# Kernel optimization log

Measured on AMD Instinct MI355X. Metric: run time of the kernel, lower is better.

The kernel has to match this reference:

```python
import jax, jax.numpy as jnp
import numpy as np

B, T, D = 4, 2048, 2048
H = 16
NOPE, ROPE, VD = 64, 64, 128
QK = NOPE + ROPE  # 128
KV_R, Q_R = 512, 1024
EPS = 1e-6
THETA = 10000.0
SCALE = 1.0 / np.sqrt(QK)


def rmsnorm(x, g):
    var = jnp.mean(jnp.square(x), axis=-1, keepdims=True)
    return x * jax.lax.rsqrt(var + EPS) * g


def rope_tables(seq_len, dim):
    inv_freq = 1.0 / (THETA ** (np.arange(0, dim, 2, dtype=np.float32) / dim))
    t = np.arange(seq_len, dtype=np.float32)
    freqs = np.outer(t, inv_freq)              # [T, dim/2]
    emb = np.concatenate([freqs, freqs], -1)   # [T, dim]
    return jnp.asarray(np.cos(emb)), jnp.asarray(np.sin(emb))


def rotate_half(x):
    x1, x2 = jnp.split(x, 2, axis=-1)
    return jnp.concatenate([-x2, x1], axis=-1)


def apply_rope(x, cos, sin):
    # x: [B,H,S,dim]; cos/sin: [S,dim] -> broadcast over B,H
    return x * cos[None, None] + rotate_half(x) * sin[None, None]


def setup_inputs() -> dict:
    key = jax.random.key(0)
    ks = jax.random.split(key, 10)
    w = lambda k, shp: jax.random.normal(k, shp, jnp.float32) * 0.02
    return {
        'x': jax.random.normal(ks[0], (B, T, D), jnp.float32),
        'w_q_down': w(ks[1], (D, Q_R)),
        'g_q_down': jnp.ones((Q_R,), jnp.float32),
        'w_q_up': w(ks[2], (Q_R, H * QK)),
        'w_kv_down': w(ks[3], (D, KV_R)),
        'g_kv_down': jnp.ones((KV_R,), jnp.float32),
        'w_k_up': w(ks[4], (KV_R, H * NOPE)),
        'w_v_up': w(ks[5], (KV_R, H * VD)),
        'w_k_rope': w(ks[6], (D, ROPE)),
        'g_q': jnp.ones((QK,), jnp.float32),
        'g_k': jnp.ones((QK,), jnp.float32),
        'w_gate': w(ks[7], (D, H * VD)),
        'w_o': w(ks[8], (H * VD, D)),
    }


def reference(x, w_q_down, g_q_down, w_q_up, w_kv_down, g_kv_down,
              w_k_up, w_v_up, w_k_rope, g_q, g_k, w_gate, w_o):
    cos, sin = rope_tables(T, ROPE)

    # Low-rank Q: down-proj -> RMSNorm -> up-proj
    q_c = rmsnorm(x @ w_q_down, g_q_down)                       # [B,T,Q_R]
    q = (q_c @ w_q_up).reshape(B, T, H, QK).transpose(0, 2, 1, 3)  # [B,H,T,QK]
    q_nope, q_rope = q[..., :NOPE], q[..., NOPE:]

    # Low-rank KV compression
    c_kv = rmsnorm(x @ w_kv_down, g_kv_down)                    # [B,S,KV_R]
    k_rope = x @ w_k_rope                                       # [B,S,ROPE]
    S = T
    k_nope = (c_kv @ w_k_up).reshape(B, S, H, NOPE).transpose(0, 2, 1, 3)
    v = (c_kv @ w_v_up).reshape(B, S, H, VD).transpose(0, 2, 1, 3)

    # Decoupled RoPE: shared k_rope broadcast over heads
    k_rope = jnp.broadcast_to(k_rope[:, None], (B, H, S, ROPE))
    q_rope = apply_rope(q_rope, cos[:T], sin[:T])
    k_rope = apply_rope(k_rope, cos[:S], sin[:S])

    q = rmsnorm(jnp.concatenate([q_nope, q_rope], -1), g_q)     # [B,H,T,QK]
    k = rmsnorm(jnp.concatenate([k_nope, k_rope], -1), g_k)     # [B,H,S,QK]

    # Causal SDPA
    scores = jnp.einsum('bhtd,bhsd->bhts', q, k) * SCALE
    mask = jnp.tril(jnp.ones((T, S), bool))
    scores = jnp.where(mask, scores, jnp.finfo(scores.dtype).min)
    attn = jax.nn.softmax(scores, axis=-1)
    out = jnp.einsum('bhts,bhsd->bhtd', attn, v)                # [B,H,T,VD]

    # Gating
    gate = (x @ w_gate).reshape(B, T, H, VD).transpose(0, 2, 1, 3)
    out = out * jax.nn.silu(gate)

    out = out.transpose(0, 2, 1, 3).reshape(B, T, H * VD)
    return out @ w_o
```

## Files before the change

kernel.cpp:

```cpp
#include <hip/hip_runtime.h>
#include <hip/hip_bf16.h>
#include <math.h>

typedef __bf16 bf16_t;
typedef __bf16 bf16x8 __attribute__((ext_vector_type(8)));
typedef float f32x4 __attribute__((ext_vector_type(4)));

#define SCALE_F 0.08838834764831845f
#define SMAX_F 14.0f

#define GLOAD_LDS16(gp, lp)                                              \
    __builtin_amdgcn_global_load_lds(                                    \
        (const __attribute__((address_space(1))) void*)(gp),             \
        (__attribute__((address_space(3))) void*)(lp), 16, 0, 0)

__global__ void k_convert(const float* __restrict__ in, bf16_t* __restrict__ out, int n) {
    int i = (blockIdx.x * 256 + threadIdx.x) * 4;
    if (i >= n) return;
    float4 f = *(const float4*)(in + i);
    out[i + 0] = (bf16_t)f.x;
    out[i + 1] = (bf16_t)f.y;
    out[i + 2] = (bf16_t)f.z;
    out[i + 3] = (bf16_t)f.w;
}

__global__ void k_transpose(const float* __restrict__ w, bf16_t* __restrict__ wt, int K, int N) {
    __shared__ float tile[32][33];
    int n0 = blockIdx.x * 32, k0 = blockIdx.y * 32;
    int tx = threadIdx.x & 31, ty = threadIdx.x >> 5;
#pragma unroll
    for (int i = 0; i < 32; i += 8)
        tile[ty + i][tx] = w[(size_t)(k0 + ty + i) * N + (n0 + tx)];
    __syncthreads();
#pragma unroll
    for (int i = 0; i < 32; i += 8)
        wt[(size_t)(n0 + ty + i) * K + (k0 + tx)] = (bf16_t)tile[tx][ty + i];
}

__global__ void k_rope_tables(float* __restrict__ cosT, float* __restrict__ sinT) {
    int idx = blockIdx.x * 256 + threadIdx.x;
    int t = idx >> 6, i = idx & 63;
    float invf = powf(10000.f, -(float)(i & 31) / 32.f);
    float ang = (float)t * invf;
    float s, c;
    sincosf(ang, &s, &c);
    cosT[idx] = c;
    sinT[idx] = s;
}

__global__ void k_rmsnorm(bf16_t* __restrict__ x, const float* __restrict__ g, int C) {
    bf16_t* p = x + (size_t)blockIdx.x * C;
    float ss = 0.f;
    for (int i = threadIdx.x; i < C; i += 256) {
        float v = (float)p[i];
        ss += v * v;
    }
#pragma unroll
    for (int m = 32; m; m >>= 1) ss += __shfl_xor(ss, m);
    __shared__ float red[4];
    if ((threadIdx.x & 63) == 0) red[threadIdx.x >> 6] = ss;
    __syncthreads();
    float tot = red[0] + red[1] + red[2] + red[3];
    float scale = rsqrtf(tot / (float)C + 1e-6f);
    for (int i = threadIdx.x; i < C; i += 256)
        p[i] = (bf16_t)((float)p[i] * scale * g[i]);
}

template <int OUTF32>
__global__ __launch_bounds__(256) void k_gemm(const bf16_t* __restrict__ A,
                                              const bf16_t* __restrict__ Bt,
                                              void* __restrict__ Cp, int M, int N, int K,
                                              size_t sA, size_t sB, size_t sC) {
    __shared__ bf16_t As[128 * 32];
    __shared__ bf16_t Bs[128 * 32];
    A += (size_t)blockIdx.z * sA;
    Bt += (size_t)blockIdx.z * sB;
    const size_t coff = (size_t)blockIdx.z * sC;
    const int bm = blockIdx.y * 128, bn = blockIdx.x * 128;
    const int tid = threadIdx.x, lane = tid & 63, wv = tid >> 6;
    const int quad = lane >> 4, l16 = lane & 15;
    const int wm = (wv >> 1) * 64, wn = (wv & 1) * 64;
    f32x4 acc[4][4] = {};
    const int sr0 = wv * 32 + (lane >> 2);
    const int scc = (lane & 3) * 8;
    bf16_t* ldsA0 = As + (wv * 2) * 512;
    bf16_t* ldsA1 = As + (wv * 2 + 1) * 512;
    bf16_t* ldsB0 = Bs + (wv * 2) * 512;
    bf16_t* ldsB1 = Bs + (wv * 2 + 1) * 512;
    const bool bok0 = (bn + sr0) < N;
    const bool bok1 = (bn + sr0 + 16) < N;
    for (int k0 = 0; k0 < K; k0 += 32) {
        const bf16_t* gA = A + (size_t)(bm + sr0) * K + k0 + scc;
        const bf16_t* gB = Bt + (size_t)(bn + sr0) * K + k0 + scc;
        GLOAD_LDS16(gA, ldsA0);
        GLOAD_LDS16(gA + (size_t)16 * K, ldsA1);
        if (bok0) GLOAD_LDS16(gB, ldsB0);
        if (bok1) GLOAD_LDS16(gB + (size_t)16 * K, ldsB1);
        __syncthreads();
        bf16x8 af[4], bfr[4];
#pragma unroll
        for (int mi = 0; mi < 4; ++mi)
            af[mi] = *(bf16x8*)(As + (wm + mi * 16 + l16) * 32 + quad * 8);
#pragma unroll
        for (int ni = 0; ni < 4; ++ni)
            bfr[ni] = *(bf16x8*)(Bs + (wn + ni * 16 + l16) * 32 + quad * 8);
#pragma unroll
        for (int mi = 0; mi < 4; ++mi)
#pragma unroll
            for (int ni = 0; ni < 4; ++ni)
                acc[mi][ni] =
                    __builtin_amdgcn_mfma_f32_16x16x32_bf16(af[mi], bfr[ni], acc[mi][ni], 0, 0, 0);
        __syncthreads();
    }
#pragma unroll
    for (int mi = 0; mi < 4; ++mi)
#pragma unroll
        for (int ni = 0; ni < 4; ++ni)
#pragma unroll
            for (int r = 0; r < 4; ++r) {
                int row = bm + wm + mi * 16 + quad * 4 + r;
                int col = bn + wn + ni * 16 + l16;
                if (col < N) {
                    if constexpr (OUTF32)
                        ((float*)Cp)[coff + (size_t)row * N + col] = acc[mi][ni][r];
                    else
                        ((bf16_t*)Cp)[coff + (size_t)row * N + col] = (bf16_t)acc[mi][ni][r];
                }
            }
}

__global__ void k_build_q(bf16_t* __restrict__ q, const float* __restrict__ g,
                          const float* __restrict__ cosT, const float* __restrict__ sinT) {
    int wid = blockIdx.x * 4 + (threadIdx.x >> 6);
    int lane = threadIdx.x & 63;
    int row = wid >> 4, h = wid & 15;
    int t = row & 2047;
    bf16_t* p = q + (size_t)row * 2048 + h * 128;
    float x0 = (float)p[lane];
    float x1 = (float)p[64 + lane];
    float xp = (float)p[64 + (lane ^ 32)];
    float c = cosT[t * 64 + lane], s = sinT[t * 64 + lane];
    float rot = (lane < 32) ? -xp : xp;
    float y1 = x1 * c + rot * s;
    float ss = x0 * x0 + y1 * y1;
#pragma unroll
    for (int m = 32; m; m >>= 1) ss += __shfl_xor(ss, m);
    float scale = rsqrtf(ss / 128.f + 1e-6f);
    p[lane] = (bf16_t)(x0 * scale * g[lane]);
    p[64 + lane] = (bf16_t)(y1 * scale * g[64 + lane]);
}

__global__ void k_build_k(const bf16_t* __restrict__ knope, const bf16_t* __restrict__ krope,
                          bf16_t* __restrict__ kout, const float* __restrict__ g,
                          const float* __restrict__ cosT, const float* __restrict__ sinT) {
    int wid = blockIdx.x * 4 + (threadIdx.x >> 6);
    int lane = threadIdx.x & 63;
    int row = wid >> 4, h = wid & 15;
    int t = row & 2047;
    float x0 = (float)knope[(size_t)row * 1024 + h * 64 + lane];
    float x1 = (float)krope[(size_t)row * 64 + lane];
    float xp = (float)krope[(size_t)row * 64 + (lane ^ 32)];
    float c = cosT[t * 64 + lane], s = sinT[t * 64 + lane];
    float rot = (lane < 32) ? -xp : xp;
    float y1 = x1 * c + rot * s;
    float ss = x0 * x0 + y1 * y1;
#pragma unroll
    for (int m = 32; m; m >>= 1) ss += __shfl_xor(ss, m);
    float scale = rsqrtf(ss / 128.f + 1e-6f);
    bf16_t* p = kout + (size_t)row * 2048 + h * 128;
    p[lane] = (bf16_t)(x0 * scale * g[lane]);
    p[64 + lane] = (bf16_t)(y1 * scale * g[64 + lane]);
}

__global__ __launch_bounds__(512, 4) void k_attn(const bf16_t* __restrict__ q,
                                                 const bf16_t* __restrict__ k,
                                                 const bf16_t* __restrict__ vT,
                                                 const bf16_t* __restrict__ gate,
                                                 bf16_t* __restrict__ o) {
    __shared__ bf16_t Ks[64 * 136];
    __shared__ bf16_t Vt[128 * 72];
    __shared__ bf16_t Ps[128 * 72];
    const int qb = (int)gridDim.x - 1 - (int)blockIdx.x;
    const int bh = blockIdx.y;
    const int b = bh >> 4, h = bh & 15;
    const int t0 = qb * 128;
    const int tid = threadIdx.x, lane = tid & 63, wv = tid >> 6;
    const int quad = lane >> 4, l16 = lane & 15;
    const int wrow = t0 + wv * 16;

    bf16x8 aq[4];
    {
        const bf16_t* qp = q + ((size_t)(b * 2048 + wrow + l16)) * 2048 + h * 128 + quad * 8;
#pragma unroll
        for (int kk = 0; kk < 4; ++kk) aq[kk] = *(const bf16x8*)(qp + kk * 32);
    }
    f32x4 oacc[8] = {};
    float l_i[4] = {0.f, 0.f, 0.f, 0.f};

    const bf16_t* vbase = vT + ((size_t)b * 2048 + (size_t)h * 128) * 2048;
    const bf16_t* kbase = k + ((size_t)b * 2048) * 2048 + h * 128;

    const int krow = tid >> 4;
    const int kcol = (tid & 15) * 8;
    const int vrow = tid >> 3;
    const int vcol = (tid & 7) * 8;

    const int nkb = 2 * qb + 2;
    bf16x8 kreg0, kreg1, vreg0, vreg1;
    {
        kreg0 = *(const bf16x8*)(kbase + (size_t)krow * 2048 + kcol);
        kreg1 = *(const bf16x8*)(kbase + (size_t)(krow + 32) * 2048 + kcol);
        vreg0 = *(const bf16x8*)(vbase + (size_t)vrow * 2048 + vcol);
        vreg1 = *(const bf16x8*)(vbase + (size_t)(vrow + 64) * 2048 + vcol);
    }
    for (int kb = 0; kb < nkb; ++kb) {
        const int s0 = kb * 64;
        __syncthreads();
        *(bf16x8*)(Ks + krow * 136 + kcol) = kreg0;
        *(bf16x8*)(Ks + (krow + 32) * 136 + kcol) = kreg1;
        *(bf16x8*)(Vt + vrow * 72 + vcol) = vreg0;
        *(bf16x8*)(Vt + (vrow + 64) * 72 + vcol) = vreg1;
        __syncthreads();
        if (kb + 1 < nkb) {
            const int sn = s0 + 64;
            kreg0 = *(const bf16x8*)(kbase + (size_t)(sn + krow) * 2048 + kcol);
            kreg1 = *(const bf16x8*)(kbase + (size_t)(sn + krow + 32) * 2048 + kcol);
            vreg0 = *(const bf16x8*)(vbase + (size_t)vrow * 2048 + sn + vcol);
            vreg1 = *(const bf16x8*)(vbase + (size_t)(vrow + 64) * 2048 + sn + vcol);
        }
        if (s0 > wrow + 15) continue;
        f32x4 sc[4] = {};
#pragma unroll
        for (int kk = 0; kk < 4; ++kk)
#pragma unroll
            for (int ni = 0; ni < 4; ++ni) {
                bf16x8 bk = *(bf16x8*)(Ks + (ni * 16 + l16) * 136 + kk * 32 + quad * 8);
                sc[ni] = __builtin_amdgcn_mfma_f32_16x16x32_bf16(aq[kk], bk, sc[ni], 0, 0, 0);
            }
        const bool diag = (s0 + 63 > wrow);
        const int trowb = wrow + quad * 4;
#pragma unroll
        for (int ni = 0; ni < 4; ++ni) {
            int scol = s0 + ni * 16 + l16;
#pragma unroll
            for (int r2 = 0; r2 < 4; ++r2) {
                float pv = __expf(sc[ni][r2] * SCALE_F - SMAX_F);
                if (diag && scol > trowb + r2) pv = 0.f;
                sc[ni][r2] = pv;
                l_i[r2] += pv;
            }
        }
#pragma unroll
        for (int ni = 0; ni < 4; ++ni)
#pragma unroll
            for (int r2 = 0; r2 < 4; ++r2)
                Ps[(wv * 16 + quad * 4 + r2) * 72 + ni * 16 + l16] = (bf16_t)sc[ni][r2];
#pragma unroll
        for (int kk = 0; kk < 2; ++kk) {
            bf16x8 ap = *(bf16x8*)(Ps + (wv * 16 + l16) * 72 + kk * 32 + quad * 8);
#pragma unroll
            for (int ni = 0; ni < 8; ++ni) {
                bf16x8 bv = *(bf16x8*)(Vt + (ni * 16 + l16) * 72 + kk * 32 + quad * 8);
                oacc[ni] = __builtin_amdgcn_mfma_f32_16x16x32_bf16(ap, bv, oacc[ni], 0, 0, 0);
            }
        }
    }
#pragma unroll
    for (int m = 8; m; m >>= 1)
#pragma unroll
        for (int r2 = 0; r2 < 4; ++r2) l_i[r2] += __shfl_xor(l_i[r2], m);
    float rl[4];
#pragma unroll
    for (int r2 = 0; r2 < 4; ++r2) rl[r2] = 1.f / l_i[r2];
#pragma unroll
    for (int ni = 0; ni < 8; ++ni) {
        int d = ni * 16 + l16;
#pragma unroll
        for (int r2 = 0; r2 < 4; ++r2) {
            int trow = wrow + quad * 4 + r2;
            size_t gi = ((size_t)(b * 2048 + trow)) * 2048 + h * 128 + d;
            float gt = (float)gate[gi];
            float sg = gt / (1.f + __expf(-gt));
            o[gi] = (bf16_t)((oacc[ni][r2] * rl[r2]) * sg);
        }
    }
}

extern "C" void kernel_launch(void* const* d_in, const int* in_sizes, int n_in,
                              void* d_out, int out_size, void* d_ws, size_t ws_size,
                              hipStream_t stream) {
    const float* x         = (const float*)d_in[0];
    const float* w_q_down  = (const float*)d_in[1];
    const float* g_q_down  = (const float*)d_in[2];
    const float* w_q_up    = (const float*)d_in[3];
    const float* w_kv_down = (const float*)d_in[4];
    const float* g_kv_down = (const float*)d_in[5];
    const float* w_k_up    = (const float*)d_in[6];
    const float* w_v_up    = (const float*)d_in[7];
    const float* w_k_rope  = (const float*)d_in[8];
    const float* g_q       = (const float*)d_in[9];
    const float* g_k       = (const float*)d_in[10];
    const float* w_gate    = (const float*)d_in[11];
    const float* w_o       = (const float*)d_in[12];
    float* out = (float*)d_out;

    char* base = (char*)d_ws;
    size_t off = 0;
    auto alloc = [&](size_t bytes) -> void* {
        void* p = base + off;
        off = (off + bytes + 255) & ~(size_t)255;
        return p;
    };
    const size_t MT = 8192;
    bf16_t* xb     = (bf16_t*)alloc(MT * 2048 * 2);
    bf16_t* wqd_t  = (bf16_t*)alloc((size_t)1024 * 2048 * 2);
    bf16_t* wqu_t  = (bf16_t*)alloc((size_t)2048 * 1024 * 2);
    bf16_t* wkvd_t = (bf16_t*)alloc((size_t)512 * 2048 * 2);
    bf16_t* wku_t  = (bf16_t*)alloc((size_t)1024 * 512 * 2);
    bf16_t* wvu_t  = (bf16_t*)alloc((size_t)2048 * 512 * 2);
    bf16_t* wkr_t  = (bf16_t*)alloc((size_t)64 * 2048 * 2);
    bf16_t* wg_t   = (bf16_t*)alloc((size_t)2048 * 2048 * 2);
    bf16_t* wo_t   = (bf16_t*)alloc((size_t)2048 * 2048 * 2);
    bf16_t* qc     = (bf16_t*)alloc(MT * 1024 * 2);
    bf16_t* ckv    = (bf16_t*)alloc(MT * 512 * 2);
    bf16_t* krope  = (bf16_t*)alloc(MT * 64 * 2);
    bf16_t* vT     = (bf16_t*)alloc(MT * 2048 * 2);
    bf16_t* gbuf   = (bf16_t*)alloc(MT * 2048 * 2);
    float* cosT    = (float*)alloc((size_t)2048 * 64 * 4);
    float* sinT    = (float*)alloc((size_t)2048 * 64 * 4);
    bf16_t* knope = qc;
    bf16_t* qbuf  = (bf16_t*)d_out;
    bf16_t* kbuf  = (bf16_t*)d_out + MT * 2048;
    bf16_t* obuf  = xb;

    k_convert<<<dim3(16384), dim3(256), 0, stream>>>(x, xb, 16777216);
    k_transpose<<<dim3(32, 64), 256, 0, stream>>>(w_q_down, wqd_t, 2048, 1024);
    k_transpose<<<dim3(64, 32), 256, 0, stream>>>(w_q_up, wqu_t, 1024, 2048);
    k_transpose<<<dim3(16, 64), 256, 0, stream>>>(w_kv_down, wkvd_t, 2048, 512);
    k_transpose<<<dim3(32, 16), 256, 0, stream>>>(w_k_up, wku_t, 512, 1024);
    k_transpose<<<dim3(64, 16), 256, 0, stream>>>(w_v_up, wvu_t, 512, 2048);
    k_transpose<<<dim3(2, 64), 256, 0, stream>>>(w_k_rope, wkr_t, 2048, 64);
    k_transpose<<<dim3(64, 64), 256, 0, stream>>>(w_gate, wg_t, 2048, 2048);
    k_transpose<<<dim3(64, 64), 256, 0, stream>>>(w_o, wo_t, 2048, 2048);
    k_rope_tables<<<dim3(512), 256, 0, stream>>>(cosT, sinT);
    k_gemm<0><<<dim3(8, 64), 256, 0, stream>>>(xb, wqd_t, qc, 8192, 1024, 2048, 0, 0, 0);
    k_rmsnorm<<<dim3(8192), 256, 0, stream>>>(qc, g_q_down, 1024);
    k_gemm<0><<<dim3(16, 64), 256, 0, stream>>>(qc, wqu_t, qbuf, 8192, 2048, 1024, 0, 0, 0);
    k_gemm<0><<<dim3(4, 64), 256, 0, stream>>>(xb, wkvd_t, ckv, 8192, 512, 2048, 0, 0, 0);
    k_rmsnorm<<<dim3(8192), 256, 0, stream>>>(ckv, g_kv_down, 512);
    k_gemm<0><<<dim3(8, 64), 256, 0, stream>>>(ckv, wku_t, knope, 8192, 1024, 512, 0, 0, 0);
    k_gemm<0><<<dim3(16, 16, 4), 256, 0, stream>>>(wvu_t, ckv, vT, 2048, 2048, 512,
                                                   0, (size_t)2048 * 512, (size_t)2048 * 2048);
    k_gemm<0><<<dim3(1, 64), 256, 0, stream>>>(xb, wkr_t, krope, 8192, 64, 2048, 0, 0, 0);
    k_gemm<0><<<dim3(16, 64), 256, 0, stream>>>(xb, wg_t, gbuf, 8192, 2048, 2048, 0, 0, 0);
    k_build_q<<<dim3(32768), 256, 0, stream>>>(qbuf, g_q, cosT, sinT);
    k_build_k<<<dim3(32768), 256, 0, stream>>>(knope, krope, kbuf, g_k, cosT, sinT);
    k_attn<<<dim3(16, 64), 512, 0, stream>>>(qbuf, kbuf, vT, gbuf, obuf);
    k_gemm<1><<<dim3(16, 64), 256, 0, stream>>>(obuf, wo_t, out, 8192, 2048, 2048, 0, 0, 0);
}
```

Baseline: 850.5 us.

## Split attention waves into 32-row by key/dim halves with XOR-swizzled LDS

The attention kernel now gives each pair of waves a 32-row query tile. The two waves split the key columns for QK^T and the value dimensions for PV, so each LDS fragment of K or V feeds two MFMAs instead of one. Padded LDS rows are replaced with an XOR swizzle to avoid bank conflicts while shrinking shared memory. The change adds an extra block barrier per key tile and an LDS reduction of the row sums across wave pairs, and each wave now computes some fully masked rows on the diagonal.

```diff
diff --git a/kernel.cpp b/kernel.cpp
--- a/kernel.cpp
+++ b/kernel.cpp
@@ -177,33 +177,40 @@
                                                  const bf16_t* __restrict__ vT,
                                                  const bf16_t* __restrict__ gate,
                                                  bf16_t* __restrict__ o) {
-    __shared__ bf16_t Ks[64 * 136];
-    __shared__ bf16_t Vt[128 * 72];
-    __shared__ bf16_t Ps[128 * 72];
+    __shared__ bf16_t Ks[64 * 128];
+    __shared__ bf16_t Vt[128 * 64];
+    __shared__ bf16_t Ps[128 * 64];
     const int qb = (int)gridDim.x - 1 - (int)blockIdx.x;
     const int bh = blockIdx.y;
     const int b = bh >> 4, h = bh & 15;
     const int t0 = qb * 128;
     const int tid = threadIdx.x, lane = tid & 63, wv = tid >> 6;
     const int quad = lane >> 4, l16 = lane & 15;
-    const int wrow = t0 + wv * 16;
-
-    bf16x8 aq[4];
-    {
-        const bf16_t* qp = q + ((size_t)(b * 2048 + wrow + l16)) * 2048 + h * 128 + quad * 8;
-#pragma unroll
-        for (int kk = 0; kk < 4; ++kk) aq[kk] = *(const bf16x8*)(qp + kk * 32);
-    }
-    f32x4 oacc[8] = {};
-    float l_i[4] = {0.f, 0.f, 0.f, 0.f};
+    const int wt = wv >> 1;
+    const int part = wv & 1;
+    const int wrow = t0 + wt * 32;
+    const int swl = (l16 & 7) << 3;
+
+    bf16x8 aq[2][4];
+#pragma unroll
+    for (int mi = 0; mi < 2; ++mi) {
+        const bf16_t* qp =
+            q + ((size_t)(b * 2048 + wrow + mi * 16 + l16)) * 2048 + h * 128 + quad * 8;
+#pragma unroll
+        for (int kk = 0; kk < 4; ++kk) aq[mi][kk] = *(const bf16x8*)(qp + kk * 32);
+    }
+    f32x4 oacc[2][4] = {};
+    float l_i[2][4] = {};
 
     const bf16_t* vbase = vT + ((size_t)b * 2048 + (size_t)h * 128) * 2048;
     const bf16_t* kbase = k + ((size_t)b * 2048) * 2048 + h * 128;
 
     const int krow = tid >> 4;
     const int kcol = (tid & 15) * 8;
+    const int kdst = krow * 128 + (kcol ^ ((krow & 7) << 3));
     const int vrow = tid >> 3;
     const int vcol = (tid & 7) * 8;
+    const int vdst = vrow * 64 + (vcol ^ ((vrow & 7) << 3));
 
     const int nkb = 2 * qb + 2;
     bf16x8 kreg0, kreg1, vreg0, vreg1;
@@ -216,10 +223,10 @@
     for (int kb = 0; kb < nkb; ++kb) {
         const int s0 = kb * 64;
         __syncthreads();
-        *(bf16x8*)(Ks + krow * 136 + kcol) = kreg0;
-        *(bf16x8*)(Ks + (krow + 32) * 136 + kcol) = kreg1;
-        *(bf16x8*)(Vt + vrow * 72 + vcol) = vreg0;
-        *(bf16x8*)(Vt + (vrow + 64) * 72 + vcol) = vreg1;
+        *(bf16x8*)(Ks + kdst) = kreg0;
+        *(bf16x8*)(Ks + kdst + 32 * 128) = kreg1;
+        *(bf16x8*)(Vt + vdst) = vreg0;
+        *(bf16x8*)(Vt + vdst + 64 * 64) = vreg1;
         __syncthreads();
         if (kb + 1 < nkb) {
             const int sn = s0 + 64;
@@ -228,61 +235,94 @@
             vreg0 = *(const bf16x8*)(vbase + (size_t)vrow * 2048 + sn + vcol);
             vreg1 = *(const bf16x8*)(vbase + (size_t)(vrow + 64) * 2048 + sn + vcol);
         }
-        if (s0 > wrow + 15) continue;
-        f32x4 sc[4] = {};
-#pragma unroll
-        for (int kk = 0; kk < 4; ++kk)
-#pragma unroll
-            for (int ni = 0; ni < 4; ++ni) {
-                bf16x8 bk = *(bf16x8*)(Ks + (ni * 16 + l16) * 136 + kk * 32 + quad * 8);
-                sc[ni] = __builtin_amdgcn_mfma_f32_16x16x32_bf16(aq[kk], bk, sc[ni], 0, 0, 0);
-            }
-        const bool diag = (s0 + 63 > wrow);
-        const int trowb = wrow + quad * 4;
-#pragma unroll
-        for (int ni = 0; ni < 4; ++ni) {
-            int scol = s0 + ni * 16 + l16;
-#pragma unroll
-            for (int r2 = 0; r2 < 4; ++r2) {
-                float pv = __expf(sc[ni][r2] * SCALE_F - SMAX_F);
-                if (diag && scol > trowb + r2) pv = 0.f;
-                sc[ni][r2] = pv;
-                l_i[r2] += pv;
+        const bool active = (s0 <= wrow + 31);
+        if (active) {
+#pragma unroll
+            for (int ni = 0; ni < 2; ++ni) {
+                f32x4 sc2[2] = {{0.f, 0.f, 0.f, 0.f}, {0.f, 0.f, 0.f, 0.f}};
+#pragma unroll
+                for (int kk = 0; kk < 4; ++kk) {
+                    bf16x8 bk = *(bf16x8*)(Ks + (part * 32 + ni * 16 + l16) * 128 +
+                                           ((kk * 32 + quad * 8) ^ swl));
+                    sc2[0] = __builtin_amdgcn_mfma_f32_16x16x32_bf16(aq[0][kk], bk, sc2[0], 0, 0, 0);
+                    sc2[1] = __builtin_amdgcn_mfma_f32_16x16x32_bf16(aq[1][kk], bk, sc2[1], 0, 0, 0);
+                }
+                const int scol = s0 + part * 32 + ni * 16 + l16;
+#pragma unroll
+                for (int mi = 0; mi < 2; ++mi) {
+                    const int trowb = wrow + mi * 16 + quad * 4;
+                    const bool dg = (s0 + part * 32 + 31) > trowb;
+                    const int prow0 = wt * 32 + mi * 16 + quad * 4;
+#pragma unroll
+                    for (int r2 = 0; r2 < 4; ++r2) {
+                        float pv = __expf(sc2[mi][r2] * SCALE_F - SMAX_F);
+                        if (dg && scol > trowb + r2) pv = 0.f;
+                        l_i[mi][r2] += pv;
+                        const int pr = prow0 + r2;
+                        Ps[pr * 64 + ((part * 32 + ni * 16 + l16) ^ ((pr & 7) << 3))] =
+                            (bf16_t)pv;
+                    }
+                }
             }
         }
-#pragma unroll
-        for (int ni = 0; ni < 4; ++ni)
-#pragma unroll
-            for (int r2 = 0; r2 < 4; ++r2)
-                Ps[(wv * 16 + quad * 4 + r2) * 72 + ni * 16 + l16] = (bf16_t)sc[ni][r2];
-#pragma unroll
-        for (int kk = 0; kk < 2; ++kk) {
-            bf16x8 ap = *(bf16x8*)(Ps + (wv * 16 + l16) * 72 + kk * 32 + quad * 8);
-#pragma unroll
-            for (int ni = 0; ni < 8; ++ni) {
-                bf16x8 bv = *(bf16x8*)(Vt + (ni * 16 + l16) * 72 + kk * 32 + quad * 8);
-                oacc[ni] = __builtin_amdgcn_mfma_f32_16x16x32_bf16(ap, bv, oacc[ni], 0, 0, 0);
+        __syncthreads();
+        if (active) {
+#pragma unroll
+            for (int kk = 0; kk < 2; ++kk) {
+                bf16x8 ap[2];
+#pragma unroll
+                for (int mi = 0; mi < 2; ++mi)
+                    ap[mi] = *(bf16x8*)(Ps + (wt * 32 + mi * 16 + l16) * 64 +
+                                        ((kk * 32 + quad * 8) ^ swl));
+#pragma unroll
+                for (int nd = 0; nd < 4; ++nd) {
+                    bf16x8 bv = *(bf16x8*)(Vt + (part * 64 + nd * 16 + l16) * 64 +
+                                           ((kk * 32 + quad * 8) ^ swl));
+#pragma unroll
+                    for (int mi = 0; mi < 2; ++mi)
+                        oacc[mi][nd] = __builtin_amdgcn_mfma_f32_16x16x32_bf16(ap[mi], bv,
+                                                                               oacc[mi][nd], 0, 0, 0);
+                }
             }
         }
     }
 #pragma unroll
     for (int m = 8; m; m >>= 1)
 #pragma unroll
-        for (int r2 = 0; r2 < 4; ++r2) l_i[r2] += __shfl_xor(l_i[r2], m);
-    float rl[4];
-#pragma unroll
-    for (int r2 = 0; r2 < 4; ++r2) rl[r2] = 1.f / l_i[r2];
-#pragma unroll
-    for (int ni = 0; ni < 8; ++ni) {
-        int d = ni * 16 + l16;
+        for (int mi = 0; mi < 2; ++mi)
+#pragma unroll
+            for (int r2 = 0; r2 < 4; ++r2) l_i[mi][r2] += __shfl_xor(l_i[mi][r2], m);
+    __syncthreads();
+    float* lbuf = (float*)Ps;
+    if (l16 == 0) {
+#pragma unroll
+        for (int mi = 0; mi < 2; ++mi)
+#pragma unroll
+            for (int r2 = 0; r2 < 4; ++r2)
+                lbuf[part * 128 + wt * 32 + mi * 16 + quad * 4 + r2] = l_i[mi][r2];
+    }
+    __syncthreads();
+    float rl[2][4];
+#pragma unroll
+    for (int mi = 0; mi < 2; ++mi)
 #pragma unroll
         for (int r2 = 0; r2 < 4; ++r2) {
-            int trow = wrow + quad * 4 + r2;
-            size_t gi = ((size_t)(b * 2048 + trow)) * 2048 + h * 128 + d;
-            float gt = (float)gate[gi];
-            float sg = gt / (1.f + __expf(-gt));
-            o[gi] = (bf16_t)((oacc[ni][r2] * rl[r2]) * sg);
+            int row = wt * 32 + mi * 16 + quad * 4 + r2;
+            rl[mi][r2] = 1.f / (lbuf[row] + lbuf[128 + row]);
         }
+#pragma unroll
+    for (int nd = 0; nd < 4; ++nd) {
+        int d = part * 64 + nd * 16 + l16;
+#pragma unroll
+        for (int mi = 0; mi < 2; ++mi)
+#pragma unroll
+            for (int r2 = 0; r2 < 4; ++r2) {
+                int trow = wrow + mi * 16 + quad * 4 + r2;
+                size_t gi = ((size_t)(b * 2048 + trow)) * 2048 + h * 128 + d;
+                float gt = (float)gate[gi];
+                float sg = gt / (1.f + __expf(-gt));
+                o[gi] = (bf16_t)((oacc[mi][nd][r2] * rl[mi][r2]) * sg);
+            }
     }
 }
 
```

Result: slower. 1.048 ms (+23.2%).

## Keep attention probabilities in registers via transposed QK^T and deepen GEMM K-step

Applied to the files above, without the earlier changes.

The attention kernel now computes S^T (K as the A operand, Q as B), so each lane holds probabilities laid out to feed the PV MFMA directly as bf16x8 registers. This removes the LDS round trip through the Ps buffer, and V is written to LDS with a permuted column order to match that register layout. The row-sum is reduced with shuffles and shared through a small LDS buffer. Separately, the GEMM loads a K-chunk of 64 per barrier pair using two LDS halves, halving the sync count at the cost of more LDS. Risks are the permuted-layout correctness, and lbuf is read without a barrier, though the write and reads stay within the same wave.

```diff
diff --git a/kernel.cpp b/kernel.cpp
--- a/kernel.cpp
+++ b/kernel.cpp
@@ -3,6 +3,7 @@
 #include <math.h>
 
 typedef __bf16 bf16_t;
+typedef __bf16 bf16x4 __attribute__((ext_vector_type(4)));
 typedef __bf16 bf16x8 __attribute__((ext_vector_type(8)));
 typedef float f32x4 __attribute__((ext_vector_type(4)));
 
@@ -71,8 +72,8 @@
                                               const bf16_t* __restrict__ Bt,
                                               void* __restrict__ Cp, int M, int N, int K,
                                               size_t sA, size_t sB, size_t sC) {
-    __shared__ bf16_t As[128 * 32];
-    __shared__ bf16_t Bs[128 * 32];
+    __shared__ bf16_t As[2][128 * 32];
+    __shared__ bf16_t Bs[2][128 * 32];
     A += (size_t)blockIdx.z * sA;
     Bt += (size_t)blockIdx.z * sB;
     const size_t coff = (size_t)blockIdx.z * sC;
@@ -83,33 +84,41 @@
     f32x4 acc[4][4] = {};
     const int sr0 = wv * 32 + (lane >> 2);
     const int scc = (lane & 3) * 8;
-    bf16_t* ldsA0 = As + (wv * 2) * 512;
-    bf16_t* ldsA1 = As + (wv * 2 + 1) * 512;
-    bf16_t* ldsB0 = Bs + (wv * 2) * 512;
-    bf16_t* ldsB1 = Bs + (wv * 2 + 1) * 512;
+    const int lo0 = (wv * 2) * 512, lo1 = (wv * 2 + 1) * 512;
     const bool bok0 = (bn + sr0) < N;
     const bool bok1 = (bn + sr0 + 16) < N;
-    for (int k0 = 0; k0 < K; k0 += 32) {
+    for (int k0 = 0; k0 < K; k0 += 64) {
         const bf16_t* gA = A + (size_t)(bm + sr0) * K + k0 + scc;
         const bf16_t* gB = Bt + (size_t)(bn + sr0) * K + k0 + scc;
-        GLOAD_LDS16(gA, ldsA0);
-        GLOAD_LDS16(gA + (size_t)16 * K, ldsA1);
-        if (bok0) GLOAD_LDS16(gB, ldsB0);
-        if (bok1) GLOAD_LDS16(gB + (size_t)16 * K, ldsB1);
+        GLOAD_LDS16(gA, As[0] + lo0);
+        GLOAD_LDS16(gA + (size_t)16 * K, As[0] + lo1);
+        GLOAD_LDS16(gA + 32, As[1] + lo0);
+        GLOAD_LDS16(gA + (size_t)16 * K + 32, As[1] + lo1);
+        if (bok0) {
+            GLOAD_LDS16(gB, Bs[0] + lo0);
+            GLOAD_LDS16(gB + 32, Bs[1] + lo0);
+        }
+        if (bok1) {
+            GLOAD_LDS16(gB + (size_t)16 * K, Bs[0] + lo1);
+            GLOAD_LDS16(gB + (size_t)16 * K + 32, Bs[1] + lo1);
+        }
         __syncthreads();
-        bf16x8 af[4], bfr[4];
-#pragma unroll
-        for (int mi = 0; mi < 4; ++mi)
-            af[mi] = *(bf16x8*)(As + (wm + mi * 16 + l16) * 32 + quad * 8);
-#pragma unroll
-        for (int ni = 0; ni < 4; ++ni)
-            bfr[ni] = *(bf16x8*)(Bs + (wn + ni * 16 + l16) * 32 + quad * 8);
-#pragma unroll
-        for (int mi = 0; mi < 4; ++mi)
+#pragma unroll
+        for (int hf = 0; hf < 2; ++hf) {
+            bf16x8 af[4], bfr[4];
+#pragma unroll
+            for (int mi = 0; mi < 4; ++mi)
+                af[mi] = *(bf16x8*)(As[hf] + (wm + mi * 16 + l16) * 32 + quad * 8);
 #pragma unroll
             for (int ni = 0; ni < 4; ++ni)
-                acc[mi][ni] =
-                    __builtin_amdgcn_mfma_f32_16x16x32_bf16(af[mi], bfr[ni], acc[mi][ni], 0, 0, 0);
+                bfr[ni] = *(bf16x8*)(Bs[hf] + (wn + ni * 16 + l16) * 32 + quad * 8);
+#pragma unroll
+            for (int mi = 0; mi < 4; ++mi)
+#pragma unroll
+                for (int ni = 0; ni < 4; ++ni)
+                    acc[mi][ni] = __builtin_amdgcn_mfma_f32_16x16x32_bf16(af[mi], bfr[ni],
+                                                                          acc[mi][ni], 0, 0, 0);
+        }
         __syncthreads();
     }
 #pragma unroll
@@ -179,7 +188,7 @@
                                                  bf16_t* __restrict__ o) {
     __shared__ bf16_t Ks[64 * 136];
     __shared__ bf16_t Vt[128 * 72];
-    __shared__ bf16_t Ps[128 * 72];
+    __shared__ float lbuf[128];
     const int qb = (int)gridDim.x - 1 - (int)blockIdx.x;
     const int bh = blockIdx.y;
     const int b = bh >> 4, h = bh & 15;
@@ -195,15 +204,19 @@
         for (int kk = 0; kk < 4; ++kk) aq[kk] = *(const bf16x8*)(qp + kk * 32);
     }
     f32x4 oacc[8] = {};
-    float l_i[4] = {0.f, 0.f, 0.f, 0.f};
+    float l_lane = 0.f;
 
     const bf16_t* vbase = vT + ((size_t)b * 2048 + (size_t)h * 128) * 2048;
     const bf16_t* kbase = k + ((size_t)b * 2048) * 2048 + h * 128;
 
     const int krow = tid >> 4;
     const int kcol = (tid & 15) * 8;
+    const int kds = krow * 136 + kcol;
     const int vrow = tid >> 3;
     const int vcol = (tid & 7) * 8;
+    const int a8 = tid & 7;
+    const int pb0 = (a8 >> 2) * 32 + (a8 & 1) * 16 + ((a8 >> 1) & 1) * 4;
+    const int vds = vrow * 72 + pb0;
 
     const int nkb = 2 * qb + 2;
     bf16x8 kreg0, kreg1, vreg0, vreg1;
@@ -216,10 +229,18 @@
     for (int kb = 0; kb < nkb; ++kb) {
         const int s0 = kb * 64;
         __syncthreads();
-        *(bf16x8*)(Ks + krow * 136 + kcol) = kreg0;
-        *(bf16x8*)(Ks + (krow + 32) * 136 + kcol) = kreg1;
-        *(bf16x8*)(Vt + vrow * 72 + vcol) = vreg0;
-        *(bf16x8*)(Vt + (vrow + 64) * 72 + vcol) = vreg1;
+        *(bf16x8*)(Ks + kds) = kreg0;
+        *(bf16x8*)(Ks + kds + 32 * 136) = kreg1;
+        {
+            bf16x4 v0lo = __builtin_shufflevector(vreg0, vreg0, 0, 1, 2, 3);
+            bf16x4 v0hi = __builtin_shufflevector(vreg0, vreg0, 4, 5, 6, 7);
+            bf16x4 v1lo = __builtin_shufflevector(vreg1, vreg1, 0, 1, 2, 3);
+            bf16x4 v1hi = __builtin_shufflevector(vreg1, vreg1, 4, 5, 6, 7);
+            *(bf16x4*)(Vt + vds) = v0lo;
+            *(bf16x4*)(Vt + vds + 8) = v0hi;
+            *(bf16x4*)(Vt + vds + 64 * 72) = v1lo;
+            *(bf16x4*)(Vt + vds + 64 * 72 + 8) = v1hi;
+        }
         __syncthreads();
         if (kb + 1 < nkb) {
             const int sn = s0 + 64;
@@ -231,57 +252,59 @@
         if (s0 > wrow + 15) continue;
         f32x4 sc[4] = {};
 #pragma unroll
-        for (int kk = 0; kk < 4; ++kk)
-#pragma unroll
-            for (int ni = 0; ni < 4; ++ni) {
-                bf16x8 bk = *(bf16x8*)(Ks + (ni * 16 + l16) * 136 + kk * 32 + quad * 8);
-                sc[ni] = __builtin_amdgcn_mfma_f32_16x16x32_bf16(aq[kk], bk, sc[ni], 0, 0, 0);
+        for (int ni = 0; ni < 4; ++ni)
+#pragma unroll
+            for (int kk = 0; kk < 4; ++kk) {
+                bf16x8 ak = *(bf16x8*)(Ks + (ni * 16 + l16) * 136 + kk * 32 + quad * 8);
+                sc[ni] = __builtin_amdgcn_mfma_f32_16x16x32_bf16(ak, aq[kk], sc[ni], 0, 0, 0);
             }
-        const bool diag = (s0 + 63 > wrow);
-        const int trowb = wrow + quad * 4;
+        const int tq = wrow + l16;
 #pragma unroll
         for (int ni = 0; ni < 4; ++ni) {
-            int scol = s0 + ni * 16 + l16;
+            const int sb = s0 + ni * 16 + quad * 4;
 #pragma unroll
             for (int r2 = 0; r2 < 4; ++r2) {
                 float pv = __expf(sc[ni][r2] * SCALE_F - SMAX_F);
-                if (diag && scol > trowb + r2) pv = 0.f;
+                if (sb + r2 > tq) pv = 0.f;
                 sc[ni][r2] = pv;
-                l_i[r2] += pv;
+                l_lane += pv;
             }
         }
-#pragma unroll
-        for (int ni = 0; ni < 4; ++ni)
-#pragma unroll
-            for (int r2 = 0; r2 < 4; ++r2)
-                Ps[(wv * 16 + quad * 4 + r2) * 72 + ni * 16 + l16] = (bf16_t)sc[ni][r2];
-#pragma unroll
-        for (int kk = 0; kk < 2; ++kk) {
-            bf16x8 ap = *(bf16x8*)(Ps + (wv * 16 + l16) * 72 + kk * 32 + quad * 8);
-#pragma unroll
-            for (int ni = 0; ni < 8; ++ni) {
-                bf16x8 bv = *(bf16x8*)(Vt + (ni * 16 + l16) * 72 + kk * 32 + quad * 8);
-                oacc[ni] = __builtin_amdgcn_mfma_f32_16x16x32_bf16(ap, bv, oacc[ni], 0, 0, 0);
-            }
-        }
-    }
-#pragma unroll
-    for (int m = 8; m; m >>= 1)
-#pragma unroll
-        for (int r2 = 0; r2 < 4; ++r2) l_i[r2] += __shfl_xor(l_i[r2], m);
+        bf16x8 pa0, pa1;
+#pragma unroll
+        for (int r2 = 0; r2 < 4; ++r2) {
+            pa0[r2] = (bf16_t)sc[0][r2];
+            pa0[4 + r2] = (bf16_t)sc[1][r2];
+            pa1[r2] = (bf16_t)sc[2][r2];
+            pa1[4 + r2] = (bf16_t)sc[3][r2];
+        }
+#pragma unroll
+        for (int nd = 0; nd < 8; ++nd) {
+            bf16x8 bv = *(bf16x8*)(Vt + (nd * 16 + l16) * 72 + quad * 8);
+            oacc[nd] = __builtin_amdgcn_mfma_f32_16x16x32_bf16(pa0, bv, oacc[nd], 0, 0, 0);
+        }
+#pragma unroll
+        for (int nd = 0; nd < 8; ++nd) {
+            bf16x8 bv = *(bf16x8*)(Vt + (nd * 16 + l16) * 72 + 32 + quad * 8);
+            oacc[nd] = __builtin_amdgcn_mfma_f32_16x16x32_bf16(pa1, bv, oacc[nd], 0, 0, 0);
+        }
+    }
+    l_lane += __shfl_xor(l_lane, 16);
+    l_lane += __shfl_xor(l_lane, 32);
+    if (quad == 0) lbuf[wv * 16 + l16] = l_lane;
     float rl[4];
 #pragma unroll
-    for (int r2 = 0; r2 < 4; ++r2) rl[r2] = 1.f / l_i[r2];
-#pragma unroll
-    for (int ni = 0; ni < 8; ++ni) {
-        int d = ni * 16 + l16;
+    for (int r2 = 0; r2 < 4; ++r2) rl[r2] = 1.f / lbuf[wv * 16 + quad * 4 + r2];
+#pragma unroll
+    for (int nd = 0; nd < 8; ++nd) {
+        int d = nd * 16 + l16;
 #pragma unroll
         for (int r2 = 0; r2 < 4; ++r2) {
             int trow = wrow + quad * 4 + r2;
             size_t gi = ((size_t)(b * 2048 + trow)) * 2048 + h * 128 + d;
             float gt = (float)gate[gi];
             float sg = gt / (1.f + __expf(-gt));
-            o[gi] = (bf16_t)((oacc[ni][r2] * rl[r2]) * sg);
+            o[gi] = (bf16_t)((oacc[nd][r2] * rl[r2]) * sg);
         }
     }
 }
```

Result: faster. 766.9 us (-9.8%).
